# Kernel tuning notes

Measured on AMD Instinct MI355X. Metric: run time of the kernel, lower is better.

## Reference

```python
import jax, jax.numpy as jnp
import numpy as np

K = 5            # local_window_size
S = K * K + 1    # num_affinity_samples = 26


def _local_indices(H, W, k):
    # Mirrors generate_local_indices: reflection-pad an arange index map and
    # unfold kxk windows -> [H*W, k*k] flat node indices.
    p = (k - 1) // 2
    idx = np.arange(H * W, dtype=np.int64).reshape(H, W)
    idx = np.pad(idx, p, mode='reflect')
    win = np.lib.stride_tricks.sliding_window_view(idx, (k, k))  # [H,W,k,k]
    return win.reshape(H * W, k * k)


def setup_inputs() -> dict:
    key = jax.random.key(0)
    ks = jax.random.split(key, 8)
    B, C, H, W = 4, 64, 128, 128
    D = 64  # kq_dim
    s = 1.0 / np.sqrt(C)
    return {
        'x': jax.random.normal(ks[0], (B, C, H, W), jnp.float32),
        'conv_w': jax.random.normal(ks[1], (D, C), jnp.float32) * s,
        'conv_b': jax.random.normal(ks[2], (D,), jnp.float32) * 0.01,
        'key_w': jax.random.normal(ks[3], (D, D), jnp.float32) * s,
        'key_b': jax.random.normal(ks[4], (D,), jnp.float32) * 0.01,
        'query_w': jax.random.normal(ks[5], (D, D), jnp.float32) * s,
        'query_b': jax.random.normal(ks[6], (D,), jnp.float32) * 0.01,
        'rand_global_inds': jax.random.randint(ks[7], (B, H * W, S - K * K), 0, H * W).astype(jnp.int64),
    }


def reference(x, conv_w, conv_b, key_w, key_b, query_w, query_b, rand_global_inds):
    B, C, H, W = x.shape
    HW = H * W
    # 1x1 conv (kq_conv): [B,C,H,W] -> [B,H,W,D]
    kq = jnp.einsum('bchw,dc->bhwd', x, conv_w) + conv_b
    # keys/query decoders (torch Linear: y = x W^T + b), flattened to [B,HW,D]
    keys = (kq @ key_w.T + key_b).reshape(B, HW, -1)
    queries = (kq @ query_w.T + query_b).reshape(B, HW, -1)
    # sample indices: 25 local window neighbors + 1 random global per node
    local = jnp.asarray(_local_indices(H, W, K))                 # [HW, 25]
    local = jnp.broadcast_to(local[None], (B, HW, K * K))
    sample_inds = jnp.concatenate([local, rand_global_inds], -1)  # [B,HW,S]
    # gather keys at sampled indices: [B,HW,S,D]
    gathered_key = jax.vmap(lambda k, idx: k[idx])(keys, sample_inds)
    # per-sample dot product with the node's own query, scaled by C^-0.5
    logits = jnp.einsum('bnd,bnsd->bns', queries, gathered_key) * (C ** -0.5)
    return logits
```

## Files before the change

### kernel.cpp

```cpp
#include <hip/hip_runtime.h>
#include <hip/hip_bf16.h>

#define HW 16384
#define NB 4

typedef __attribute__((ext_vector_type(8))) short bf16x8;
typedef __attribute__((ext_vector_type(4))) float f32x4;

__device__ __forceinline__ float blo(unsigned u) { return __uint_as_float(u << 16); }
__device__ __forceinline__ float bhi(unsigned u) { return __uint_as_float(u & 0xffff0000u); }


__global__ __launch_bounds__(256) void combine_weights(
    const float* __restrict__ conv_w, const float* __restrict__ conv_b,
    const float* __restrict__ key_w, const float* __restrict__ key_b,
    const float* __restrict__ query_w, const float* __restrict__ query_b,
    ushort* __restrict__ Wb, float* __restrict__ bout) {
    int t = threadIdx.x, bx = blockIdx.x;
    int sel = bx >> 4, d0 = (bx & 15) * 4;
    const float* Wm = sel ? query_w : key_w;
    float scale = sel ? 0.125f : 1.0f;
    int dd = t >> 6, c = t & 63;
    const float* wrow = Wm + (d0 + dd) * 64;
    float acc = 0.f;
    #pragma unroll
    for (int k = 0; k < 64; ++k) acc = fmaf(wrow[k], conv_w[k * 64 + c], acc);
    __hip_bfloat16 h = __float2bfloat16(acc * scale);
    Wb[(sel * 64 + d0 + dd) * 64 + c] = *(ushort*)&h;
    if (t < 4) {
        const float* wr2 = Wm + (d0 + t) * 64;
        float bacc = 0.f;
        #pragma unroll
        for (int k = 0; k < 64; ++k) bacc = fmaf(wr2[k], conv_b[k], bacc);
        bacc += (sel ? query_b : key_b)[d0 + t];
        bout[sel * 64 + d0 + t] = bacc * scale;
    }
}

__global__ __launch_bounds__(256) void gemm_kq(
    const float* __restrict__ x, const ushort* __restrict__ W,
    const float* __restrict__ bias, ushort* __restrict__ keys,
    ushort* __restrict__ queries) {
    __shared__ ushort xs[128 * 64];
    __shared__ ushort epi[2 * 128 * 64];
    __shared__ float bs[128];
    int t = threadIdx.x;
    int b = blockIdx.x >> 7;
    int n0 = (blockIdx.x & 127) << 7;

    if (t < 128) bs[t] = bias[t];
    {
        int c0 = (t >> 5) * 8, nb = (t & 31) * 4;
        const float* xp = x + ((size_t)(b * 64 + c0)) * HW + n0 + nb;
        float4 v[8];
        #pragma unroll
        for (int r = 0; r < 8; ++r) v[r] = *(const float4*)(xp + (size_t)r * HW);
        int chunk = c0 >> 3;
        #pragma unroll
        for (int nn = 0; nn < 4; ++nn) {
            unsigned u[4];
            #pragma unroll
            for (int cc = 0; cc < 4; ++cc) {
                float lo = ((const float*)&v[2 * cc])[nn];
                float hi = ((const float*)&v[2 * cc + 1])[nn];
                __hip_bfloat162 h2 = __float22bfloat162_rn(make_float2(lo, hi));
                u[cc] = *(unsigned*)&h2;
            }
            int row = nb + nn;
            *(uint4*)((char*)xs + row * 128 + ((chunk ^ (row & 7)) << 4)) =
                make_uint4(u[0], u[1], u[2], u[3]);
        }
    }
    __syncthreads();

    int l = t & 63, w = t >> 6;
    int ncol = l & 15, kg = l >> 4;
    int nhalf = w & 1, dhalf = w >> 1;

    bf16x8 Bf[4][2];
    #pragma unroll
    for (int nt = 0; nt < 4; ++nt) {
        int row = nhalf * 64 + nt * 16 + ncol;
        #pragma unroll
        for (int half = 0; half < 2; ++half)
            Bf[nt][half] = *(bf16x8*)((char*)xs + row * 128 + (((half * 4 + kg) ^ (row & 7)) << 4));
    }

    f32x4 acc[4][4];
    #pragma unroll
    for (int dt = 0; dt < 4; ++dt)
        #pragma unroll
        for (int nt = 0; nt < 4; ++nt) acc[dt][nt] = (f32x4){0.f, 0.f, 0.f, 0.f};

    #pragma unroll
    for (int dt = 0; dt < 4; ++dt) {
        const bf16x8* arow = (const bf16x8*)(W + ((dhalf * 64 + dt * 16 + ncol)) * 64 + kg * 8);
        bf16x8 A0 = arow[0];
        bf16x8 A1 = arow[4];
        #pragma unroll
        for (int nt = 0; nt < 4; ++nt) {
            acc[dt][nt] = __builtin_amdgcn_mfma_f32_16x16x32_bf16(A0, Bf[nt][0], acc[dt][nt], 0, 0, 0);
            acc[dt][nt] = __builtin_amdgcn_mfma_f32_16x16x32_bf16(A1, Bf[nt][1], acc[dt][nt], 0, 0, 0);
        }
    }

    #pragma unroll
    for (int dt = 0; dt < 4; ++dt) {
        int dbase = dt * 16 + kg * 4;
        float4 bb = *(float4*)&bs[dhalf * 64 + dbase];
        #pragma unroll
        for (int nt = 0; nt < 4; ++nt) {
            int nl = nhalf * 64 + nt * 16 + ncol;
            f32x4 a = acc[dt][nt];
            __hip_bfloat162 lo2 = __float22bfloat162_rn(make_float2(a[0] + bb.x, a[1] + bb.y));
            __hip_bfloat162 hi2 = __float22bfloat162_rn(make_float2(a[2] + bb.z, a[3] + bb.w));
            *(uint2*)((char*)epi + dhalf * 16384 + nl * 128 +
                      (((dbase >> 3) ^ (nl & 7)) << 4) + ((dbase & 4) << 1)) =
                make_uint2(*(unsigned*)&lo2, *(unsigned*)&hi2);
        }
    }
    __syncthreads();
    #pragma unroll
    for (int i = 0; i < 8; ++i) {
        int u = i * 256 + t;
        int arr = u >> 10;
        int row = (u >> 3) & 127, ch = u & 7;
        uint4 v = *(uint4*)((char*)epi + arr * 16384 + row * 128 + ((ch ^ (row & 7)) << 4));
        ushort* dst = arr ? queries : keys;
        *(uint4*)(dst + (((size_t)(b * HW + n0 + row)) << 6) + ch * 8) = v;
    }
}

#define DOT(s_, idxn_) do {                                                   \
    const uint4* kp = (const uint4*)(kb_ + ((size_t)(idxn_) << 6));           \
    uint4 ka = kp[0], kc = kp[1];                                             \
    float a = 0.f;                                                            \
    a = fmaf(blo(ka.x), qf[0], a);  a = fmaf(bhi(ka.x), qf[1], a);            \
    a = fmaf(blo(ka.y), qf[2], a);  a = fmaf(bhi(ka.y), qf[3], a);            \
    a = fmaf(blo(ka.z), qf[4], a);  a = fmaf(bhi(ka.z), qf[5], a);            \
    a = fmaf(blo(ka.w), qf[6], a);  a = fmaf(bhi(ka.w), qf[7], a);            \
    a = fmaf(blo(kc.x), qf[8], a);  a = fmaf(bhi(kc.x), qf[9], a);            \
    a = fmaf(blo(kc.y), qf[10], a); a = fmaf(bhi(kc.y), qf[11], a);           \
    a = fmaf(blo(kc.z), qf[12], a); a = fmaf(bhi(kc.z), qf[13], a);           \
    a = fmaf(blo(kc.w), qf[14], a); a = fmaf(bhi(kc.w), qf[15], a);           \
    a += __shfl_xor(a, 1);                                                    \
    a += __shfl_xor(a, 2);                                                    \
    if (j == 0) res[n_loc * 26 + (s_)] = a;                                   \
} while (0)

#define SAMP(s_, dy_, dx_) do {                                               \
    int ry = y + (dy_);                                                       \
    if ((dy_) < 0) ry = (ry < 0) ? -ry : ry;                                  \
    if ((dy_) > 0) ry = (ry > 127) ? 254 - ry : ry;                           \
    int rx = xq + (dx_);                                                      \
    if ((dx_) < 0) rx = (rx < 0) ? -rx : rx;                                  \
    if ((dx_) > 0) rx = (rx > 127) ? 254 - rx : rx;                           \
    DOT(s_, (ry << 7) + rx);                                                  \
} while (0)

__global__ __launch_bounds__(256) void affinity(
    const ushort* __restrict__ keys, const ushort* __restrict__ queries,
    const int* __restrict__ rnd, float* __restrict__ out) {
    __shared__ float res[416];
    int t = threadIdx.x;
    int b = blockIdx.x >> 10;
    int n0 = (blockIdx.x & 1023) << 4;

    int j = t & 3;
    int g = t >> 2;
    int n_loc = g & 15;
    int sb = g >> 4;
    int n = n0 + n_loc;

    const uint4* qp = (const uint4*)(queries + (((size_t)(b * HW + n)) << 6) + j * 16);
    uint4 qa = qp[0], qb = qp[1];
    float qf[16];
    qf[0] = blo(qa.x); qf[1] = bhi(qa.x); qf[2] = blo(qa.y); qf[3] = bhi(qa.y);
    qf[4] = blo(qa.z); qf[5] = bhi(qa.z); qf[6] = blo(qa.w); qf[7] = bhi(qa.w);
    qf[8] = blo(qb.x); qf[9] = bhi(qb.x); qf[10] = blo(qb.y); qf[11] = bhi(qb.y);
    qf[12] = blo(qb.z); qf[13] = bhi(qb.z); qf[14] = blo(qb.w); qf[15] = bhi(qb.w);

    int y = n >> 7, xq = n & 127;
    const ushort* kb_ = keys + (((size_t)b * HW) << 6) + j * 16;

    switch (sb) {
    case 0:
        SAMP(0, -2, -2); SAMP(4, -2, 2);  SAMP(8, -1, 1);  SAMP(12, 0, 0);
        SAMP(16, 1, -1); SAMP(20, 2, -2); SAMP(24, 2, 2);
        break;
    case 1: {
        SAMP(1, -2, -1); SAMP(5, -1, -2); SAMP(9, -1, 2);  SAMP(13, 0, 1);
        SAMP(17, 1, 0);  SAMP(21, 2, -1);
        int rix = rnd[b * HW + n];
        DOT(25, rix);
        break;
    }
    case 2:
        SAMP(2, -2, 0);  SAMP(6, -1, -1); SAMP(10, 0, -2); SAMP(14, 0, 2);
        SAMP(18, 1, 1);  SAMP(22, 2, 0);
        break;
    default:
        SAMP(3, -2, 1);  SAMP(7, -1, 0);  SAMP(11, 0, -1); SAMP(15, 1, -2);
        SAMP(19, 1, 2);  SAMP(23, 2, 1);
        break;
    }
    __syncthreads();
    size_t ob = ((size_t)(b * HW + n0)) * 26;
    out[ob + t] = res[t];
    if (t < 160) out[ob + 256 + t] = res[256 + t];
}

extern "C" void kernel_launch(void* const* d_in, const int* in_sizes, int n_in,
                              void* d_out, int out_size, void* d_ws, size_t ws_size,
                              hipStream_t stream) {
    const float* x       = (const float*)d_in[0];
    const float* conv_w  = (const float*)d_in[1];
    const float* conv_b  = (const float*)d_in[2];
    const float* key_w   = (const float*)d_in[3];
    const float* key_b   = (const float*)d_in[4];
    const float* query_w = (const float*)d_in[5];
    const float* query_b = (const float*)d_in[6];
    const int*   rnd     = (const int*)d_in[7];
    float* out = (float*)d_out;

    ushort* Wb    = (ushort*)d_ws;
    float*  biasp = (float*)((char*)d_ws + 16384);
    ushort* keys  = (ushort*)((char*)d_ws + 32768);
    ushort* quer  = keys + (size_t)NB * HW * 64;

    combine_weights<<<32, 256, 0, stream>>>(conv_w, conv_b, key_w, key_b,
                                            query_w, query_b, Wb, biasp);
    gemm_kq<<<NB * (HW / 128), 256, 0, stream>>>(x, Wb, biasp, keys, quer);
    affinity<<<NB * (HW / 16), 256, 0, stream>>>(keys, quer, rnd, out);
}
```

Measured before the change: 34.42 us.

## Store keys/queries in fp32, drop LDS epilogue, swizzle affinity block order

Result: slower. 56.49 us (+64.1%).

```diff
diff --git a/kernel.cpp b/kernel.cpp
--- a/kernel.cpp
+++ b/kernel.cpp
@@ -6,9 +6,6 @@
 
 typedef __attribute__((ext_vector_type(8))) short bf16x8;
 typedef __attribute__((ext_vector_type(4))) float f32x4;
-
-__device__ __forceinline__ float blo(unsigned u) { return __uint_as_float(u << 16); }
-__device__ __forceinline__ float bhi(unsigned u) { return __uint_as_float(u & 0xffff0000u); }
 
 
 __global__ __launch_bounds__(256) void combine_weights(
@@ -39,10 +36,9 @@
 
 __global__ __launch_bounds__(256) void gemm_kq(
     const float* __restrict__ x, const ushort* __restrict__ W,
-    const float* __restrict__ bias, ushort* __restrict__ keys,
-    ushort* __restrict__ queries) {
+    const float* __restrict__ bias, float* __restrict__ keys,
+    float* __restrict__ queries) {
     __shared__ ushort xs[128 * 64];
-    __shared__ ushort epi[2 * 128 * 64];
     __shared__ float bs[128];
     int t = threadIdx.x;
     int b = blockIdx.x >> 7;
@@ -104,45 +100,34 @@
         }
     }
 
+    float* dst = dhalf ? queries : keys;
     #pragma unroll
     for (int dt = 0; dt < 4; ++dt) {
         int dbase = dt * 16 + kg * 4;
         float4 bb = *(float4*)&bs[dhalf * 64 + dbase];
         #pragma unroll
         for (int nt = 0; nt < 4; ++nt) {
-            int nl = nhalf * 64 + nt * 16 + ncol;
+            int n = n0 + nhalf * 64 + nt * 16 + ncol;
             f32x4 a = acc[dt][nt];
-            __hip_bfloat162 lo2 = __float22bfloat162_rn(make_float2(a[0] + bb.x, a[1] + bb.y));
-            __hip_bfloat162 hi2 = __float22bfloat162_rn(make_float2(a[2] + bb.z, a[3] + bb.w));
-            *(uint2*)((char*)epi + dhalf * 16384 + nl * 128 +
-                      (((dbase >> 3) ^ (nl & 7)) << 4) + ((dbase & 4) << 1)) =
-                make_uint2(*(unsigned*)&lo2, *(unsigned*)&hi2);
+            *(float4*)(dst + (((size_t)(b * HW + n)) << 6) + dbase) =
+                make_float4(a[0] + bb.x, a[1] + bb.y, a[2] + bb.z, a[3] + bb.w);
         }
     }
-    __syncthreads();
-    #pragma unroll
-    for (int i = 0; i < 8; ++i) {
-        int u = i * 256 + t;
-        int arr = u >> 10;
-        int row = (u >> 3) & 127, ch = u & 7;
-        uint4 v = *(uint4*)((char*)epi + arr * 16384 + row * 128 + ((ch ^ (row & 7)) << 4));
-        ushort* dst = arr ? queries : keys;
-        *(uint4*)(dst + (((size_t)(b * HW + n0 + row)) << 6) + ch * 8) = v;
-    }
 }
 
 #define DOT(s_, idxn_) do {                                                   \
-    const uint4* kp = (const uint4*)(kb_ + ((size_t)(idxn_) << 6));           \
-    uint4 ka = kp[0], kc = kp[1];                                             \
-    float a = 0.f;                                                            \
-    a = fmaf(blo(ka.x), qf[0], a);  a = fmaf(bhi(ka.x), qf[1], a);            \
-    a = fmaf(blo(ka.y), qf[2], a);  a = fmaf(bhi(ka.y), qf[3], a);            \
-    a = fmaf(blo(ka.z), qf[4], a);  a = fmaf(bhi(ka.z), qf[5], a);            \
-    a = fmaf(blo(ka.w), qf[6], a);  a = fmaf(bhi(ka.w), qf[7], a);            \
-    a = fmaf(blo(kc.x), qf[8], a);  a = fmaf(bhi(kc.x), qf[9], a);            \
-    a = fmaf(blo(kc.y), qf[10], a); a = fmaf(bhi(kc.y), qf[11], a);           \
-    a = fmaf(blo(kc.z), qf[12], a); a = fmaf(bhi(kc.z), qf[13], a);           \
-    a = fmaf(blo(kc.w), qf[14], a); a = fmaf(bhi(kc.w), qf[15], a);           \
+    const float4* kp = (const float4*)(kb_ + ((size_t)(idxn_) << 6));         \
+    float4 k0 = kp[0], k1 = kp[1], k2 = kp[2], k3 = kp[3];                    \
+    float a0, a1;                                                             \
+    a0 = k0.x * qf[0];               a1 = k0.y * qf[1];                       \
+    a0 = fmaf(k0.z, qf[2], a0);      a1 = fmaf(k0.w, qf[3], a1);              \
+    a0 = fmaf(k1.x, qf[4], a0);      a1 = fmaf(k1.y, qf[5], a1);              \
+    a0 = fmaf(k1.z, qf[6], a0);      a1 = fmaf(k1.w, qf[7], a1);              \
+    a0 = fmaf(k2.x, qf[8], a0);      a1 = fmaf(k2.y, qf[9], a1);              \
+    a0 = fmaf(k2.z, qf[10], a0);     a1 = fmaf(k2.w, qf[11], a1);             \
+    a0 = fmaf(k3.x, qf[12], a0);     a1 = fmaf(k3.y, qf[13], a1);             \
+    a0 = fmaf(k3.z, qf[14], a0);     a1 = fmaf(k3.w, qf[15], a1);             \
+    float a = a0 + a1;                                                        \
     a += __shfl_xor(a, 1);                                                    \
     a += __shfl_xor(a, 2);                                                    \
     if (j == 0) res[n_loc * 26 + (s_)] = a;                                   \
@@ -159,12 +144,14 @@
 } while (0)
 
 __global__ __launch_bounds__(256) void affinity(
-    const ushort* __restrict__ keys, const ushort* __restrict__ queries,
+    const float* __restrict__ keys, const float* __restrict__ queries,
     const int* __restrict__ rnd, float* __restrict__ out) {
     __shared__ float res[416];
     int t = threadIdx.x;
-    int b = blockIdx.x >> 10;
-    int n0 = (blockIdx.x & 1023) << 4;
+    int bid = blockIdx.x;
+    int swz = (bid & 7) * 512 + (bid >> 3);
+    int b = swz >> 10;
+    int n0 = (swz & 1023) << 4;
 
     int j = t & 3;
     int g = t >> 2;
@@ -172,16 +159,13 @@
     int sb = g >> 4;
     int n = n0 + n_loc;
 
-    const uint4* qp = (const uint4*)(queries + (((size_t)(b * HW + n)) << 6) + j * 16);
-    uint4 qa = qp[0], qb = qp[1];
-    float qf[16];
-    qf[0] = blo(qa.x); qf[1] = bhi(qa.x); qf[2] = blo(qa.y); qf[3] = bhi(qa.y);
-    qf[4] = blo(qa.z); qf[5] = bhi(qa.z); qf[6] = blo(qa.w); qf[7] = bhi(qa.w);
-    qf[8] = blo(qb.x); qf[9] = bhi(qb.x); qf[10] = blo(qb.y); qf[11] = bhi(qb.y);
-    qf[12] = blo(qb.z); qf[13] = bhi(qb.z); qf[14] = blo(qb.w); qf[15] = bhi(qb.w);
+    const float4* qp = (const float4*)(queries + (((size_t)(b * HW + n)) << 6) + j * 16);
+    float4 q0 = qp[0], q1 = qp[1], q2 = qp[2], q3 = qp[3];
+    float qf[16] = {q0.x, q0.y, q0.z, q0.w, q1.x, q1.y, q1.z, q1.w,
+                    q2.x, q2.y, q2.z, q2.w, q3.x, q3.y, q3.z, q3.w};
 
     int y = n >> 7, xq = n & 127;
-    const ushort* kb_ = keys + (((size_t)b * HW) << 6) + j * 16;
+    const float* kb_ = keys + (((size_t)b * HW) << 6) + j * 16;
 
     switch (sb) {
     case 0:
@@ -225,8 +209,8 @@
 
     ushort* Wb    = (ushort*)d_ws;
     float*  biasp = (float*)((char*)d_ws + 16384);
-    ushort* keys  = (ushort*)((char*)d_ws + 32768);
-    ushort* quer  = keys + (size_t)NB * HW * 64;
+    float*  keys  = (float*)((char*)d_ws + 32768);
+    float*  quer  = keys + (size_t)NB * HW * 64;
 
     combine_weights<<<32, 256, 0, stream>>>(conv_w, conv_b, key_w, key_b,
                                             query_w, query_b, Wb, biasp);
```
